# Optimization experiments

Hardware: AMD Instinct MI355X
Metric: run time of the kernel (lower is better)

## Reference

```python
import jax, jax.numpy as jnp
import numpy as np

B, S, E, D, A = 32, 2048, 1024, 1024, 1024


def setup_inputs() -> dict:
    key = jax.random.key(0)
    k1, k2, k3, k4, k5, k6, k7, k8 = jax.random.split(key, 8)
    # Kaiming-uniform-ish init scales (values don't matter for correctness)
    def lin(kw, kb, fan_in, fan_out):
        bound = 1.0 / np.sqrt(fan_in)
        W = jax.random.uniform(kw, (fan_out, fan_in), minval=-bound, maxval=bound, dtype=jnp.float32)
        b = jax.random.uniform(kb, (fan_out,), minval=-bound, maxval=bound, dtype=jnp.float32)
        return W, b
    W_enc, b_enc = lin(k1, k2, E, A)
    W_dec, b_dec = lin(k3, k4, D, A)
    W_v, b_v = lin(k5, k6, A, 1)
    encoder_out = jax.random.normal(k7, (B, S, E), dtype=jnp.float32)
    decoder_hidden = jax.random.normal(k8, (B, D), dtype=jnp.float32)
    return {
        "encoder_out": encoder_out,
        "decoder_hidden": decoder_hidden,
        "W_enc": W_enc, "b_enc": b_enc,
        "W_dec": W_dec, "b_dec": b_dec,
        "W_v": W_v, "b_v": b_v,
    }


def reference(encoder_out, decoder_hidden, W_enc, b_enc, W_dec, b_dec, W_v, b_v):
    # encoder_proj: [B, S, A]
    encoder_proj = jnp.einsum('bse,ae->bsa', encoder_out, W_enc) + b_enc
    # decoder_proj: [B, 1, A]
    decoder_proj = (jnp.einsum('bd,ad->ba', decoder_hidden, W_dec) + b_dec)[:, None, :]
    # scores: [B, S] (V projects attention_dim -> 1)
    scores = jnp.einsum('bsa,a->bs', jnp.tanh(encoder_proj + decoder_proj), W_v[0]) + b_v[0]
    alpha = jax.nn.softmax(scores, axis=1)  # [B, S]
    context = jnp.einsum('bse,bs->be', encoder_out, alpha)  # [B, E]
    return (context, alpha)
```

## Files before the change

### kernel.cpp

```cpp
#include <hip/hip_runtime.h>

typedef unsigned short ushort_t;
typedef __attribute__((ext_vector_type(8))) short short8;
typedef __attribute__((ext_vector_type(4))) float f32x4;


__device__ __forceinline__ ushort_t f2bf(float f) {
    unsigned u = __builtin_bit_cast(unsigned, f);
    u += 0x7fffu + ((u >> 16) & 1u);
    return (ushort_t)(u >> 16);
}

__device__ __forceinline__ float bf2f(ushort_t h) {
    unsigned u = ((unsigned)h) << 16;
    return __builtin_bit_cast(float, u);
}

__device__ __forceinline__ float tanh_fast(float x) {
    float e = __expf(2.0f * x);
    float r = __builtin_amdgcn_rcpf(e + 1.0f);
    return __builtin_fmaf(-2.0f, r, 1.0f);
}

__device__ __forceinline__ void gld16(const ushort_t* g, ushort_t* lds) {
    __builtin_amdgcn_global_load_lds(
        (const __attribute__((address_space(1))) unsigned int*)g,
        (__attribute__((address_space(3))) unsigned int*)lds, 16, 0, 0);
}

#define WAITCNT_VM8 (8 | (7 << 4) | (15 << 8))
#define WAITCNT_VM0 (0 | (7 << 4) | (15 << 8))


__global__ __launch_bounds__(256) void k_front(const float* __restrict__ enc,
                                               const float* __restrict__ Wenc,
                                               const float* __restrict__ dh,
                                               const float* __restrict__ Wd,
                                               const float* __restrict__ bd,
                                               const float* __restrict__ be,
                                               ushort_t* __restrict__ encB,
                                               ushort_t* __restrict__ wencB,
                                               float* __restrict__ dproj,
                                               float4* __restrict__ scores4) {
    const int bx = blockIdx.x;
    const int t = threadIdx.x;
    if (bx < 8192) {
        int i = bx * 256 + t;
        for (; i < 17055744; i += 2097152) {
            if (i < 16777216) {
                float4 v = ((const float4*)enc)[i];
                ushort4 o;
                o.x = f2bf(v.x); o.y = f2bf(v.y); o.z = f2bf(v.z); o.w = f2bf(v.w);
                ((ushort4*)encB)[i] = o;
            } else if (i < 17039360) {
                int j = i - 16777216;
                float4 v = ((const float4*)Wenc)[j];
                ushort4 o;
                o.x = f2bf(v.x); o.y = f2bf(v.y); o.z = f2bf(v.z); o.w = f2bf(v.w);
                ((ushort4*)wencB)[j] = o;
            } else {
                scores4[i - 17039360] = (float4){0.f, 0.f, 0.f, 0.f};
            }
        }
    } else {
        int wid = (bx - 8192) * 4 + (t >> 6);
        int lane = t & 63;
        int a = wid & 1023, b = wid >> 10;
        const float4* x = (const float4*)(dh + (size_t)b * 1024);
        const float4* wrow = (const float4*)(Wd + (size_t)a * 1024);
        float s = 0.f;
#pragma unroll
        for (int it = 0; it < 4; ++it) {
            int c = it * 64 + lane;
            float4 xv = x[c], wv = wrow[c];
            s += xv.x * wv.x + xv.y * wv.y + xv.z * wv.z + xv.w * wv.w;
        }
#pragma unroll
        for (int o = 1; o < 64; o <<= 1) s += __shfl_xor(s, o, 64);
        if (lane == 0) dproj[b * 1024 + a] = s + bd[a] + be[a];
    }
}


__global__ __launch_bounds__(256, 2) void k_gemm_scores(const ushort_t* __restrict__ A,
                                                        const ushort_t* __restrict__ Bm,
                                                        const float* __restrict__ dproj,
                                                        const float* __restrict__ Wv,
                                                        float* __restrict__ scores) {
    __shared__ __align__(16) ushort_t At[2][8192];
    __shared__ __align__(16) ushort_t Bt[2][8192];

    const int tid = threadIdx.x;
    const int lane = tid & 63;
    const int w = tid >> 6;
    const int wm = w >> 1, wn = w & 1;

    const int blk = blockIdx.x;
    const int q2 = blk >> 3;
    const int blkN = q2 & 7;
    const int blkM = (blk & 7) + ((q2 >> 3) << 3);
    const long long arow0 = (long long)blkM * 128;
    const int brow0 = blkN * 128;

    const int sr = lane >> 3;
    const int sgrp = lane & 7;
    const int c8s = sgrp ^ sr;

    const int q = lane >> 4;
    const int ml = lane & 15;

    const ushort_t* ga = A + (arow0 + w * 32 + sr) * 1024 + c8s * 8;
    const ushort_t* gb = Bm + (long long)(brow0 + w * 32 + sr) * 1024 + c8s * 8;

    f32x4 acc[4][4];
#pragma unroll
    for (int i = 0; i < 4; ++i)
#pragma unroll
        for (int jj = 0; jj < 4; ++jj) acc[i][jj] = (f32x4){0.f, 0.f, 0.f, 0.f};

#pragma unroll
    for (int j = 0; j < 4; ++j) {
        gld16(ga + j * 8192, &At[0][(w * 4 + j) * 512]);
        gld16(gb + j * 8192, &Bt[0][(w * 4 + j) * 512]);
    }

    for (int it = 0; it < 16; ++it) {
        const int cur = it & 1;
        if (it < 15) {
            const ushort_t* ga2 = ga + (it + 1) * 64;
            const ushort_t* gb2 = gb + (it + 1) * 64;
#pragma unroll
            for (int j = 0; j < 4; ++j) {
                gld16(ga2 + j * 8192, &At[cur ^ 1][(w * 4 + j) * 512]);
                gld16(gb2 + j * 8192, &Bt[cur ^ 1][(w * 4 + j) * 512]);
            }
            __builtin_amdgcn_s_waitcnt(WAITCNT_VM8);
        } else {
            __builtin_amdgcn_s_waitcnt(WAITCNT_VM0);
        }
        __atomic_signal_fence(__ATOMIC_ACQ_REL);
        __builtin_amdgcn_s_barrier();
        __atomic_signal_fence(__ATOMIC_ACQ_REL);

#pragma unroll
        for (int kk = 0; kk < 2; ++kk) {
            const int kb = kk * 4;
            short8 af[4], bfr[4];
#pragma unroll
            for (int i = 0; i < 4; ++i) {
                int row = wm * 64 + i * 16 + ml;
                int slot = (kb + q) ^ (row & 7);
                af[i] = *(const short8*)&At[cur][row * 64 + slot * 8];
                int col = wn * 64 + i * 16 + ml;
                int slotb = (kb + q) ^ (col & 7);
                bfr[i] = *(const short8*)&Bt[cur][col * 64 + slotb * 8];
            }
#pragma unroll
            for (int i = 0; i < 4; ++i)
#pragma unroll
                for (int jj = 0; jj < 4; ++jj)
                    acc[i][jj] = __builtin_amdgcn_mfma_f32_16x16x32_bf16(
                        af[i], bfr[jj], acc[i][jj], 0, 0, 0);
        }
        __atomic_signal_fence(__ATOMIC_ACQ_REL);
        __builtin_amdgcn_s_barrier();
        __atomic_signal_fence(__ATOMIC_ACQ_REL);
    }

    const int bb = blkM >> 4;
#pragma unroll
    for (int i = 0; i < 4; ++i) {
        float rs[4] = {0.f, 0.f, 0.f, 0.f};
#pragma unroll
        for (int jj = 0; jj < 4; ++jj) {
            int a = blkN * 128 + wn * 64 + jj * 16 + ml;
            float dp = dproj[bb * 1024 + a];
            float wv = Wv[a];
            f32x4 v = acc[i][jj];
            rs[0] += wv * tanh_fast(v.x + dp);
            rs[1] += wv * tanh_fast(v.y + dp);
            rs[2] += wv * tanh_fast(v.z + dp);
            rs[3] += wv * tanh_fast(v.w + dp);
        }
#pragma unroll
        for (int r = 0; r < 4; ++r)
#pragma unroll
            for (int o = 1; o < 16; o <<= 1) rs[r] += __shfl_xor(rs[r], o, 64);
        if (ml == 0) {
            long long m0 = arow0 + wm * 64 + i * 16 + q * 4;
            atomicAdd(&scores[m0 + 0], rs[0]);
            atomicAdd(&scores[m0 + 1], rs[1]);
            atomicAdd(&scores[m0 + 2], rs[2]);
            atomicAdd(&scores[m0 + 3], rs[3]);
        }
    }
}


__global__ __launch_bounds__(256) void k_softmax(const float* __restrict__ scores,
                                                 float* __restrict__ out) {
    const int b = blockIdx.x, t = threadIdx.x;
    const int lane = t & 63, w = t >> 6;
    __shared__ float red[4];
#pragma unroll
    for (int j = t; j < 1024; j += 256) out[b * 1024 + j] = 0.f;
    float v[8];
#pragma unroll
    for (int j = 0; j < 8; ++j) v[j] = scores[b * 2048 + j * 256 + t];
    float mx = v[0];
#pragma unroll
    for (int j = 1; j < 8; ++j) mx = fmaxf(mx, v[j]);
#pragma unroll
    for (int o = 1; o < 64; o <<= 1) mx = fmaxf(mx, __shfl_xor(mx, o, 64));
    if (lane == 0) red[w] = mx;
    __syncthreads();
    mx = fmaxf(fmaxf(red[0], red[1]), fmaxf(red[2], red[3]));
    float s = 0.f;
#pragma unroll
    for (int j = 0; j < 8; ++j) { v[j] = __expf(v[j] - mx); s += v[j]; }
#pragma unroll
    for (int o = 1; o < 64; o <<= 1) s += __shfl_xor(s, o, 64);
    __syncthreads();
    if (lane == 0) red[w] = s;
    __syncthreads();
    s = red[0] + red[1] + red[2] + red[3];
    float inv = 1.0f / s;
#pragma unroll
    for (int j = 0; j < 8; ++j) out[32768 + b * 2048 + j * 256 + t] = v[j] * inv;
}


__global__ __launch_bounds__(256) void k_context(const ushort_t* __restrict__ encB,
                                                 const float* __restrict__ alpha,
                                                 float* __restrict__ out) {
    const int b = blockIdx.x, ec = blockIdx.y, sc = blockIdx.z, t = threadIdx.x;
    const int l = t & 31, g = t >> 5;
    __shared__ float al[256];
    __shared__ f32x4 part[8][33];
    al[t] = alpha[b * 2048 + sc * 256 + t];
    __syncthreads();
    const ushort_t* ep = encB + ((size_t)(b * 2048 + sc * 256 + g * 32)) * 1024 + ec * 128 + l * 4;
    const float* ag = &al[g * 32];
    f32x4 acc = (f32x4){0.f, 0.f, 0.f, 0.f};
#pragma unroll 4
    for (int s = 0; s < 32; ++s) {
        ushort4 ev = *(const ushort4*)(ep + (size_t)s * 1024);
        float a = ag[s];
        acc.x += a * bf2f(ev.x);
        acc.y += a * bf2f(ev.y);
        acc.z += a * bf2f(ev.z);
        acc.w += a * bf2f(ev.w);
    }
    part[g][l] = acc;
    __syncthreads();
    if (t < 32) {
        f32x4 s = part[0][t];
#pragma unroll
        for (int gg = 1; gg < 8; ++gg) {
            f32x4 p = part[gg][t];
            s.x += p.x; s.y += p.y; s.z += p.z; s.w += p.w;
        }
        float* dst = out + b * 1024 + ec * 128 + t * 4;
        atomicAdd(dst + 0, s.x);
        atomicAdd(dst + 1, s.y);
        atomicAdd(dst + 2, s.z);
        atomicAdd(dst + 3, s.w);
    }
}


extern "C" void kernel_launch(void* const* d_in, const int* in_sizes, int n_in,
                              void* d_out, int out_size, void* d_ws, size_t ws_size,
                              hipStream_t stream) {
    const float* enc  = (const float*)d_in[0];
    const float* dh   = (const float*)d_in[1];
    const float* Wenc = (const float*)d_in[2];
    const float* benc = (const float*)d_in[3];
    const float* Wdec = (const float*)d_in[4];
    const float* bdec = (const float*)d_in[5];
    const float* Wv   = (const float*)d_in[6];
    float* out = (float*)d_out;

    char* ws = (char*)d_ws;
    ushort_t* encB  = (ushort_t*)ws;
    ushort_t* wencB = (ushort_t*)(ws + 134217728ull);
    float* dproj    = (float*)(ws + 134217728ull + 2097152ull);
    float* scores   = (float*)(ws + 134217728ull + 2097152ull + 131072ull);

    k_front<<<16384, 256, 0, stream>>>(enc, Wenc, dh, Wdec, bdec, benc,
                                       encB, wencB, dproj, (float4*)scores);
    k_gemm_scores<<<4096, 256, 0, stream>>>(encB, wencB, dproj, Wv, scores);
    k_softmax<<<32, 256, 0, stream>>>(scores, out);
    k_context<<<dim3(32, 8, 8), 256, 0, stream>>>(encB, out + 32768, out);
}
```

Measured before the change: 598.6 us.

## Enlarge GEMM tile to 256x128 and drop LDS double buffering

The scores GEMM now uses a 256x128 output tile per block with 8x4 MFMA accumulators per wave, which halves the block count and raises reuse of the W_enc tile. The double-buffered LDS prefetch pipeline is replaced by a single buffer that loads, waits on all outstanding loads, then computes. The dproj and W_v loads are also hoisted out of the epilogue loop. The larger tile cuts global traffic per FLOP, but the loss of load/compute overlap and higher register pressure may hurt latency hiding.

```diff
diff --git a/kernel.cpp b/kernel.cpp
--- a/kernel.cpp
+++ b/kernel.cpp
@@ -27,9 +27,6 @@
         (const __attribute__((address_space(1))) unsigned int*)g,
         (__attribute__((address_space(3))) unsigned int*)lds, 16, 0, 0);
 }
-
-#define WAITCNT_VM8 (8 | (7 << 4) | (15 << 8))
-#define WAITCNT_VM0 (0 | (7 << 4) | (15 << 8))
 
 
 __global__ __launch_bounds__(256) void k_front(const float* __restrict__ enc,
@@ -87,8 +84,8 @@
                                                         const float* __restrict__ dproj,
                                                         const float* __restrict__ Wv,
                                                         float* __restrict__ scores) {
-    __shared__ __align__(16) ushort_t At[2][8192];
-    __shared__ __align__(16) ushort_t Bt[2][8192];
+    __shared__ __align__(16) ushort_t At[256 * 64];
+    __shared__ __align__(16) ushort_t Bt[128 * 64];
 
     const int tid = threadIdx.x;
     const int lane = tid & 63;
@@ -99,7 +96,7 @@
     const int q2 = blk >> 3;
     const int blkN = q2 & 7;
     const int blkM = (blk & 7) + ((q2 >> 3) << 3);
-    const long long arow0 = (long long)blkM * 128;
+    const long long arow0 = (long long)blkM * 256;
     const int brow0 = blkN * 128;
 
     const int sr = lane >> 3;
@@ -109,85 +106,76 @@
     const int q = lane >> 4;
     const int ml = lane & 15;
 
-    const ushort_t* ga = A + (arow0 + w * 32 + sr) * 1024 + c8s * 8;
+    const ushort_t* ga = A + (arow0 + w * 64 + sr) * 1024 + c8s * 8;
     const ushort_t* gb = Bm + (long long)(brow0 + w * 32 + sr) * 1024 + c8s * 8;
 
-    f32x4 acc[4][4];
-#pragma unroll
-    for (int i = 0; i < 4; ++i)
+    f32x4 acc[8][4];
+#pragma unroll
+    for (int i = 0; i < 8; ++i)
 #pragma unroll
         for (int jj = 0; jj < 4; ++jj) acc[i][jj] = (f32x4){0.f, 0.f, 0.f, 0.f};
 
-#pragma unroll
-    for (int j = 0; j < 4; ++j) {
-        gld16(ga + j * 8192, &At[0][(w * 4 + j) * 512]);
-        gld16(gb + j * 8192, &Bt[0][(w * 4 + j) * 512]);
-    }
-
-    for (int it = 0; it < 16; ++it) {
-        const int cur = it & 1;
-        if (it < 15) {
-            const ushort_t* ga2 = ga + (it + 1) * 64;
-            const ushort_t* gb2 = gb + (it + 1) * 64;
-#pragma unroll
-            for (int j = 0; j < 4; ++j) {
-                gld16(ga2 + j * 8192, &At[cur ^ 1][(w * 4 + j) * 512]);
-                gld16(gb2 + j * 8192, &Bt[cur ^ 1][(w * 4 + j) * 512]);
-            }
-            __builtin_amdgcn_s_waitcnt(WAITCNT_VM8);
-        } else {
-            __builtin_amdgcn_s_waitcnt(WAITCNT_VM0);
-        }
-        __atomic_signal_fence(__ATOMIC_ACQ_REL);
-        __builtin_amdgcn_s_barrier();
-        __atomic_signal_fence(__ATOMIC_ACQ_REL);
+    for (int k0 = 0; k0 < 1024; k0 += 64) {
+        __syncthreads();
+#pragma unroll
+        for (int j = 0; j < 8; ++j)
+            gld16(ga + j * 8192, &At[(w * 8 + j) * 512]);
+#pragma unroll
+        for (int j = 0; j < 4; ++j)
+            gld16(gb + j * 8192, &Bt[(w * 4 + j) * 512]);
+        ga += 64; gb += 64;
+        __builtin_amdgcn_s_waitcnt(0);
+        __syncthreads();
 
 #pragma unroll
         for (int kk = 0; kk < 2; ++kk) {
             const int kb = kk * 4;
-            short8 af[4], bfr[4];
-#pragma unroll
-            for (int i = 0; i < 4; ++i) {
-                int row = wm * 64 + i * 16 + ml;
-                int slot = (kb + q) ^ (row & 7);
-                af[i] = *(const short8*)&At[cur][row * 64 + slot * 8];
-                int col = wn * 64 + i * 16 + ml;
-                int slotb = (kb + q) ^ (col & 7);
-                bfr[i] = *(const short8*)&Bt[cur][col * 64 + slotb * 8];
+            const int slot = (kb + q) ^ (ml & 7);
+            short8 af[8], bfr[4];
+#pragma unroll
+            for (int i = 0; i < 8; ++i) {
+                int row = wm * 128 + i * 16 + ml;
+                af[i] = *(const short8*)&At[row * 64 + slot * 8];
             }
 #pragma unroll
-            for (int i = 0; i < 4; ++i)
+            for (int jj = 0; jj < 4; ++jj) {
+                int col = wn * 64 + jj * 16 + ml;
+                bfr[jj] = *(const short8*)&Bt[col * 64 + slot * 8];
+            }
+#pragma unroll
+            for (int i = 0; i < 8; ++i)
 #pragma unroll
                 for (int jj = 0; jj < 4; ++jj)
                     acc[i][jj] = __builtin_amdgcn_mfma_f32_16x16x32_bf16(
                         af[i], bfr[jj], acc[i][jj], 0, 0, 0);
         }
-        __atomic_signal_fence(__ATOMIC_ACQ_REL);
-        __builtin_amdgcn_s_barrier();
-        __atomic_signal_fence(__ATOMIC_ACQ_REL);
-    }
-
-    const int bb = blkM >> 4;
-#pragma unroll
-    for (int i = 0; i < 4; ++i) {
+    }
+
+    const int bb = blkM >> 3;
+    float dp[4], wv[4];
+#pragma unroll
+    for (int jj = 0; jj < 4; ++jj) {
+        int a = blkN * 128 + wn * 64 + jj * 16 + ml;
+        dp[jj] = dproj[bb * 1024 + a];
+        wv[jj] = Wv[a];
+    }
+#pragma unroll
+    for (int i = 0; i < 8; ++i) {
         float rs[4] = {0.f, 0.f, 0.f, 0.f};
 #pragma unroll
         for (int jj = 0; jj < 4; ++jj) {
-            int a = blkN * 128 + wn * 64 + jj * 16 + ml;
-            float dp = dproj[bb * 1024 + a];
-            float wv = Wv[a];
             f32x4 v = acc[i][jj];
-            rs[0] += wv * tanh_fast(v.x + dp);
-            rs[1] += wv * tanh_fast(v.y + dp);
-            rs[2] += wv * tanh_fast(v.z + dp);
-            rs[3] += wv * tanh_fast(v.w + dp);
+            rs[0] += wv[jj] * tanh_fast(v.x + dp[jj]);
+            rs[1] += wv[jj] * tanh_fast(v.y + dp[jj]);
+            rs[2] += wv[jj] * tanh_fast(v.z + dp[jj]);
+            rs[3] += wv[jj] * tanh_fast(v.w + dp[jj]);
         }
 #pragma unroll
         for (int r = 0; r < 4; ++r)
 #pragma unroll
             for (int o = 1; o < 16; o <<= 1) rs[r] += __shfl_xor(rs[r], o, 64);
         if (ml == 0) {
-            long long m0 = arow0 + wm * 64 + i * 16 + q * 4;
+            long long m0 = arow0 + wm * 128 + i * 16 + q * 4;
             atomicAdd(&scores[m0 + 0], rs[0]);
             atomicAdd(&scores[m0 + 1], rs[1]);
             atomicAdd(&scores[m0 + 2], rs[2]);
@@ -289,7 +277,7 @@
 
     k_front<<<16384, 256, 0, stream>>>(enc, Wenc, dh, Wdec, bdec, benc,
                                        encB, wencB, dproj, (float4*)scores);
-    k_gemm_scores<<<4096, 256, 0, stream>>>(encB, wencB, dproj, Wv, scores);
+    k_gemm_scores<<<2048, 256, 0, stream>>>(encB, wencB, dproj, Wv, scores);
     k_softmax<<<32, 256, 0, stream>>>(scores, out);
     k_context<<<dim3(32, 8, 8), 256, 0, stream>>>(encB, out + 32768, out);
 }
```

After: 550.5 us. 1.09x faster.
